# Performance work log

Measured on AMD Instinct MI355X. Metric: run time of the kernel, lower is better.

Reference implementation:

```python
import jax, jax.numpy as jnp
import numpy as np

B = 65536        # batch of class observations
NUM_CLASSES = 100
D = 128          # embedding_latent_dim / MLP width
H = 64           # rnn_hidden_dim == vq_embedding_dim (must match when use_vq)
K = 512          # vq_num_embeddings
S = 16           # num_splines
A = 6            # spline_action_dim
SQUISH = 0.2
BETA = 0.25      # vq commitment cost


def setup_inputs() -> dict:
    key = jax.random.key(0)
    ks = jax.random.split(key, 32)
    g = lambda i, shape, s=0.05: jax.random.normal(ks[i], shape, jnp.float32) * s
    return dict(
        obs=jax.random.randint(ks[0], (B,), 0, NUM_CLASSES, dtype=jnp.int32),
        embed=g(1, (NUM_CLASSES, D)),
        W1=g(2, (D, D)), b1=jnp.zeros((D,), jnp.float32),
        W2=g(3, (D, D)), b2=jnp.zeros((D,), jnp.float32),
        W3=g(4, (D, D)), b3=jnp.zeros((D,), jnp.float32),
        Wc=g(5, (D, H)), bc=jnp.zeros((H,), jnp.float32),      # carry_init
        Wi=g(6, (D, H)), bi=jnp.zeros((H,), jnp.float32),      # SimpleCell input dense
        Wh=g(7, (H, H)),                                       # SimpleCell recurrent (no bias)
        vq_emb=g(8, (K, H)),                                   # VQ codebook
        Wm=g(9, (H, A)), bm=jnp.zeros((A,), jnp.float32),      # actor mean head
        Ws=g(10, (H, A)), bs=jnp.zeros((A,), jnp.float32),     # actor scale head
        Vw1=g(11, (D, D)), vb1=jnp.zeros((D,), jnp.float32),
        Vw2=g(12, (D, D)), vb2=jnp.zeros((D,), jnp.float32),
        Vw3=g(13, (D, 32)), vb3=jnp.zeros((32,), jnp.float32),
        Vw4=g(14, (32, 1)), vb4=jnp.zeros((1,), jnp.float32),
    )


def reference(obs, embed, W1, b1, W2, b2, W3, b3, Wc, bc, Wi, bi, Wh, vq_emb,
              Wm, bm, Ws, bs, Vw1, vb1, Vw2, vb2, Vw3, vb3, Vw4, vb4):
    # class embedding + ReLU MLP trunk
    z = embed[obs]                                # (B, D)
    z = jax.nn.relu(z @ W1 + b1)
    z = jax.nn.relu(z @ W2 + b2)
    z = jax.nn.relu(z @ W3 + b3)

    carry0 = z @ Wc + bc                          # (B, H) initial RNN carry
    emb_sq = jnp.sum(vq_emb ** 2, axis=1)         # (K,) precomputed codebook norms

    def step(carry, _):
        # SimpleCell: h = tanh(Dense(inputs) + Dense_h(carry)); inputs = z each step
        h = jnp.tanh(z @ Wi + bi + carry @ Wh)    # (B, H)
        # VQ nearest-neighbor lookup
        d = jnp.sum(h ** 2, axis=1, keepdims=True) - 2.0 * (h @ vq_emb.T) + emb_sq  # (B, K)
        idx = jnp.argmin(d, axis=1)               # (B,)
        quant = jnp.take(vq_emb, idx, axis=0)     # (B, H) == one_hot(idx) @ vq_emb
        q = h + jax.lax.stop_gradient(quant - h)  # straight-through estimator
        e_loss = jnp.mean((jax.lax.stop_gradient(q) - h) ** 2)
        q_loss = jnp.mean((q - jax.lax.stop_gradient(h)) ** 2)
        vq_loss_i = q_loss + BETA * e_loss
        # spline heads (use_tanh_last=False -> sigmoid, temp=1)
        am = jax.nn.sigmoid(q @ Wm + bm)                    # (B, A)
        sd = jax.nn.sigmoid(q @ Ws + bs) * SQUISH + 1e-8    # (B, A)
        return q, (am, sd, vq_loss_i, idx)

    _, (ams, sds, losses, idxs) = jax.lax.scan(step, carry0, None, length=S)
    # (S, B, A) -> (B, S*A), matching concatenate along axis 1 in step order
    actor_mean = jnp.transpose(ams, (1, 0, 2)).reshape(B, S * A)
    actor_scale_diag = jnp.transpose(sds, (1, 0, 2)).reshape(B, S * A)

    # critic MLP (tanh activations)
    c = jnp.tanh(z @ Vw1 + vb1)
    c = jnp.tanh(c @ Vw2 + vb2)
    c = jnp.tanh(c @ Vw3 + vb3)
    critic = jnp.squeeze(c @ Vw4 + vb4, axis=-1)  # (B,)

    total_vq_loss = jnp.sum(losses)
    return actor_mean, actor_scale_diag, critic, total_vq_loss, idxs
```

## Files before the change

kernel.cpp:

```cpp
#include <hip/hip_runtime.h>
#include <cmath>


#define D_ 128
#define H_ 64
#define K_ 512
#define S_ 16
#define B_ 65536
#define NTBL_ 64
#define NH_ 16

#define OAM   ((size_t)0)
#define OSD   ((size_t)(B_ * 96))
#define OCRIT ((size_t)(2 * B_ * 96))
#define OLOSS ((size_t)(2 * B_ * 96 + B_))
#define OIDX  ((size_t)(2 * B_ * 96 + B_ + 1))

#define WS_CLIDX  0
#define WS_CLAM   (WS_CLIDX + 128 * 16)
#define WS_CLSD   (WS_CLAM + 128 * 96)
#define WS_CLCR   (WS_CLSD + 128 * 96)
#define WS_CLLOSS (WS_CLCR + 128)

__device__ float g_vqwh[K_ * H_];
__device__ float g_am8[K_ * 8];
__device__ float g_sd8[K_ * 8];
__device__ float g_embsq[K_];
__device__ int   g_cntp[NH_ * 128];
__device__ int   g_tflag = 0;

typedef const __attribute__((address_space(1))) void GASV;
typedef __attribute__((address_space(3))) void LASV;
__device__ __forceinline__ void gll16(const void* g, void* l)
{
    __builtin_amdgcn_global_load_lds((GASV*)g, (LASV*)l, 16, 0, 0);
}

template <int N4>
__device__ __forceinline__ void dma_lin(float4* __restrict__ dst,
                                        const float4* __restrict__ src,
                                        int wid, int lane)
{
    constexpr int PER = N4 / 8;
#pragma unroll
    for (int j = 0; j < PER; j += 64) {
        const int f = wid * PER + j;
        gll16(src + f + lane, dst + f);
    }
}

template <int CTRL>
__device__ __forceinline__ void dpp_min(float& bD, int& bK)
{
    const int od_i = __builtin_amdgcn_update_dpp(
        __float_as_int(bD), __float_as_int(bD), CTRL, 0xF, 0xF, false);
    const int ok = __builtin_amdgcn_update_dpp(bK, bK, CTRL, 0xF, 0xF, false);
    const float od = __int_as_float(od_i);
    if (od < bD || (od == bD && ok < bK)) { bD = od; bK = ok; }
}

__global__ __launch_bounds__(512)
__attribute__((amdgpu_waves_per_eu(2, 2)))
void class_kernel(
    const int* __restrict__ obs, int nclass,
    const float* __restrict__ embed,
    const float* __restrict__ W1, const float* __restrict__ b1,
    const float* __restrict__ W2, const float* __restrict__ b2,
    const float* __restrict__ W3, const float* __restrict__ b3,
    const float* __restrict__ Wc, const float* __restrict__ bc,
    const float* __restrict__ Wi, const float* __restrict__ bi,
    const float* __restrict__ Wh,
    const float* __restrict__ Wm, const float* __restrict__ bm,
    const float* __restrict__ Wsw, const float* __restrict__ bs,
    const float* __restrict__ Vw1, const float* __restrict__ vb1,
    const float* __restrict__ Vw2, const float* __restrict__ vb2,
    const float* __restrict__ Vw3, const float* __restrict__ vb3,
    const float* __restrict__ Vw4, const float* __restrict__ vb4,
    const float* __restrict__ vq_emb,
    float* __restrict__ clam, float* __restrict__ clsd,
    float* __restrict__ clcr, float* __restrict__ clidx,
    float* __restrict__ clloss)
{
    extern __shared__ float4 dyn4[];
    float* __restrict__ Af    = reinterpret_cast<float*>(dyn4);
    float* __restrict__ Bf    = reinterpret_cast<float*>(dyn4 + 4096);
    float* __restrict__ vqwhL = reinterpret_cast<float*>(dyn4);
    __shared__ float zA[128], zB[128];
    __shared__ float psum[512];
    __shared__ float psumC[256];
    __shared__ float t1s[64], c0s[64], c3s[32];
    __shared__ float vw4s[32] __attribute__((aligned(16)));
    __shared__ float Wh_s[64 * 64] __attribute__((aligned(16)));
    __shared__ float hcand[2][4][64] __attribute__((aligned(16)));
    __shared__ float rDp[2][4] __attribute__((aligned(16)));
    __shared__ int   rKp[2][4] __attribute__((aligned(16)));
    __shared__ int   gk_s[16];
    __shared__ float gd_s[16];
    __shared__ float hh_s[16];

    const int bx   = blockIdx.x;
    const int tid  = threadIdx.x;
    const int lane = tid & 63;
    const int wid  = tid >> 6;

    if (bx < NTBL_) {
        float* __restrict__ er = reinterpret_cast<float*>(dyn4) + wid * 64;
        const int k = bx * 8 + wid;
        er[lane] = vq_emb[k * 64 + lane];
        __syncthreads();

        float acc = 0.f;
#pragma unroll 16
        for (int dd = 0; dd < 64; ++dd)
            acc = fmaf(er[dd], Wh[dd * 64 + lane], acc);
        g_vqwh[k * 64 + lane] = acc;

        float sq = er[lane] * er[lane];
#pragma unroll
        for (int m = 1; m < 64; m <<= 1) sq += __shfl_xor(sq, m);
        if (lane == 0) g_embsq[k] = sq;

        if (lane < 8) {
            float vm = 0.f, vs = 0.f;
            if (lane < 6) {
                vm = bm[lane];
                vs = bs[lane];
#pragma unroll 16
                for (int dd = 0; dd < 64; ++dd) {
                    vm = fmaf(er[dd], Wm[dd * 6 + lane], vm);
                    vs = fmaf(er[dd], Wsw[dd * 6 + lane], vs);
                }
                vm = 1.f / (1.f + expf(-vm));
                vs = 1.f / (1.f + expf(-vs)) * 0.2f + 1e-8f;
            }
            g_am8[k * 8 + lane] = vm;
            g_sd8[k * 8 + lane] = vs;
        }
        __syncthreads();
        if (tid == 0) {
            __threadfence();
            __hip_atomic_fetch_add(&g_tflag, 1, __ATOMIC_RELEASE,
                                   __HIP_MEMORY_SCOPE_AGENT);
        }
        return;
    }

    if (bx < NTBL_ + NH_) {
        int* __restrict__ hsh = reinterpret_cast<int*>(psum);
        if (tid < 128) hsh[tid] = 0;
        __syncthreads();
        const int hb = bx - NTBL_;
        for (int i = hb * 512 + tid; i < B_; i += NH_ * 512)
            atomicAdd(&hsh[obs[i]], 1);
        __syncthreads();
        if (tid < 128) g_cntp[hb * 128 + tid] = hsh[tid];
        return;
    }

    const int c = bx - NTBL_ - NH_;
    const float4* __restrict__ vq4   = reinterpret_cast<const float4*>(vq_emb);
    const float4* __restrict__ vqwh4 =
        reinterpret_cast<const float4*>(&g_vqwh[0]);

    const int j128 = tid & 127;
    const int q4   = tid >> 7;

    dma_lin<4096>(dyn4, reinterpret_cast<const float4*>(W1), wid, lane);
    if (tid < 128) zA[tid] = embed[c * 128 + tid];
    __syncthreads();

#define DENSE128(SRCW, ZSRC, ZDST, BIAS, ACT)                                  \
    {                                                                          \
        float a0 = 0.f, a1 = 0.f, a2 = 0.f, a3 = 0.f;                          \
        const int i0 = q4 * 32;                                                \
        _Pragma("unroll 8")                                                    \
        for (int ii = 0; ii < 32; ii += 4) {                                   \
            a0 = fmaf(ZSRC[i0 + ii + 0], SRCW[(i0 + ii + 0) * 128 + j128], a0);\
            a1 = fmaf(ZSRC[i0 + ii + 1], SRCW[(i0 + ii + 1) * 128 + j128], a1);\
            a2 = fmaf(ZSRC[i0 + ii + 2], SRCW[(i0 + ii + 2) * 128 + j128], a2);\
            a3 = fmaf(ZSRC[i0 + ii + 3], SRCW[(i0 + ii + 3) * 128 + j128], a3);\
        }                                                                      \
        psum[q4 * 128 + j128] = (a0 + a1) + (a2 + a3);                         \
    }                                                                          \
    __syncthreads();                                                           \
    if (tid < 128) {                                                           \
        float v = BIAS[tid] + ((psum[tid] + psum[128 + tid]) +                 \
                               (psum[256 + tid] + psum[384 + tid]));           \
        ZDST[tid] = ACT;                                                       \
    }                                                                          \
    __syncthreads();

    dma_lin<4096>(dyn4 + 4096, reinterpret_cast<const float4*>(W2), wid, lane);
    DENSE128(Af, zA, zB, b1, fmaxf(v, 0.f))

    dma_lin<4096>(dyn4, reinterpret_cast<const float4*>(W3), wid, lane);
    DENSE128(Bf, zB, zA, b2, fmaxf(v, 0.f))

    dma_lin<2048>(dyn4 + 4096, reinterpret_cast<const float4*>(Wi), wid, lane);
    dma_lin<2048>(dyn4 + 6144, reinterpret_cast<const float4*>(Wc), wid, lane);
    DENSE128(Af, zA, zB, b3, fmaxf(v, 0.f))

    if (tid == 0) {
        while (__hip_atomic_load(&g_tflag, __ATOMIC_RELAXED,
                                 __HIP_MEMORY_SCOPE_AGENT) < NTBL_)
            __builtin_amdgcn_s_sleep(2);
    }
    __syncthreads();

    dma_lin<4096>(dyn4, vqwh4, wid, lane);
    dma_lin<1024>(reinterpret_cast<float4*>(Wh_s),
                  reinterpret_cast<const float4*>(Wh), wid, lane);
    if (wid < 4) {
        const int jj = lane;
        const int qq = wid;
        const int i0 = qq * 32;
        {
            float a0 = 0.f, a1 = 0.f, a2 = 0.f, a3 = 0.f;
#pragma unroll 8
            for (int ii = 0; ii < 32; ii += 4) {
                a0 = fmaf(zB[i0 + ii + 0], Bf[(i0 + ii + 0) * 64 + jj], a0);
                a1 = fmaf(zB[i0 + ii + 1], Bf[(i0 + ii + 1) * 64 + jj], a1);
                a2 = fmaf(zB[i0 + ii + 2], Bf[(i0 + ii + 2) * 64 + jj], a2);
                a3 = fmaf(zB[i0 + ii + 3], Bf[(i0 + ii + 3) * 64 + jj], a3);
            }
            psum[qq * 64 + jj] = (a0 + a1) + (a2 + a3);
        }
        {
            const float* __restrict__ Wsrc = Bf + 8192;
            float a0 = 0.f, a1 = 0.f, a2 = 0.f, a3 = 0.f;
#pragma unroll 8
            for (int ii = 0; ii < 32; ii += 4) {
                a0 = fmaf(zB[i0 + ii + 0], Wsrc[(i0 + ii + 0) * 64 + jj], a0);
                a1 = fmaf(zB[i0 + ii + 1], Wsrc[(i0 + ii + 1) * 64 + jj], a1);
                a2 = fmaf(zB[i0 + ii + 2], Wsrc[(i0 + ii + 2) * 64 + jj], a2);
                a3 = fmaf(zB[i0 + ii + 3], Wsrc[(i0 + ii + 3) * 64 + jj], a3);
            }
            psum[256 + qq * 64 + jj] = (a0 + a1) + (a2 + a3);
        }
    } else {
        const int u = tid - 256;
        const int j = u & 127;
        const int hf = u >> 7;
        const int i0 = 64 * hf;
        float ca0 = 0.f, ca1 = 0.f, ca2 = 0.f, ca3 = 0.f;
#pragma unroll 8
        for (int ii = 0; ii < 64; ii += 4) {
            ca0 = fmaf(zB[i0 + ii + 0], Vw1[(i0 + ii + 0) * 128 + j], ca0);
            ca1 = fmaf(zB[i0 + ii + 1], Vw1[(i0 + ii + 1) * 128 + j], ca1);
            ca2 = fmaf(zB[i0 + ii + 2], Vw1[(i0 + ii + 2) * 128 + j], ca2);
            ca3 = fmaf(zB[i0 + ii + 3], Vw1[(i0 + ii + 3) * 128 + j], ca3);
        }
        psumC[u] = (ca0 + ca1) + (ca2 + ca3);
    }
    __syncthreads();

    dma_lin<4096>(dyn4 + 4096, vqwh4 + 4096, wid, lane);
    if (tid < 64) {
        t1s[tid] = bi[tid] + ((psum[tid] + psum[64 + tid]) +
                              (psum[128 + tid] + psum[192 + tid]));
    } else if (tid < 128) {
        const int j = tid - 64;
        c0s[j] = bc[j] + ((psum[256 + j] + psum[320 + j]) +
                          (psum[384 + j] + psum[448 + j]));
    } else if (tid < 160) {
        vw4s[tid - 128] = Vw4[tid - 128];
    } else if (tid >= 256 && tid < 384) {
        const int u = tid - 256;
        zA[u] = tanhf(vb1[u] + psumC[u] + psumC[128 + u]);
    }
    __syncthreads();

    float4 cb[16], cb2[16];
    float esq = 0.f, esq2 = 0.f;
    if (wid < 4) {
        const int j = lane;
#pragma unroll
        for (int qq2 = 0; qq2 < 2; ++qq2) {
            const int q = wid + 4 * qq2;
            float a0 = 0.f, a1 = 0.f;
            const int i0 = q * 8;
#pragma unroll
            for (int ii = 0; ii < 8; ii += 2) {
                a0 = fmaf(c0s[i0 + ii + 0], Wh_s[(i0 + ii + 0) * 64 + j], a0);
                a1 = fmaf(c0s[i0 + ii + 1], Wh_s[(i0 + ii + 1) * 64 + j], a1);
            }
            psum[q * 64 + j] = a0 + a1;
        }
        const float4* __restrict__ r1 = vq4 + (size_t)tid * 16;
        const float4* __restrict__ r2 = vq4 + (size_t)(tid + 256) * 16;
#pragma unroll
        for (int d4 = 0; d4 < 16; ++d4) { cb[d4] = r1[d4]; cb2[d4] = r2[d4]; }
#pragma unroll
        for (int d4 = 0; d4 < 16; ++d4) {
            asm volatile("" : "+v"(cb[d4].x), "+v"(cb[d4].y),
                              "+v"(cb[d4].z), "+v"(cb[d4].w));
            asm volatile("" : "+v"(cb2[d4].x), "+v"(cb2[d4].y),
                              "+v"(cb2[d4].z), "+v"(cb2[d4].w));
        }
        esq  = g_embsq[tid];
        esq2 = g_embsq[tid + 256];
    } else {
        const int u = tid - 256;
        const int j = u & 127;
        const int hf = u >> 7;
        const int i0 = 64 * hf;
        float ca0 = 0.f, ca1 = 0.f, ca2 = 0.f, ca3 = 0.f;
#pragma unroll 8
        for (int ii = 0; ii < 64; ii += 4) {
            ca0 = fmaf(zA[i0 + ii + 0], Vw2[(i0 + ii + 0) * 128 + j], ca0);
            ca1 = fmaf(zA[i0 + ii + 1], Vw2[(i0 + ii + 1) * 128 + j], ca1);
            ca2 = fmaf(zA[i0 + ii + 2], Vw2[(i0 + ii + 2) * 128 + j], ca2);
            ca3 = fmaf(zA[i0 + ii + 3], Vw2[(i0 + ii + 3) * 128 + j], ca3);
        }
        psumC[u] = (ca0 + ca1) + (ca2 + ca3);
    }
    __syncthreads();

    if (tid < 64) {
        float a = 0.f;
#pragma unroll
        for (int q = 0; q < 8; ++q) a += psum[q * 64 + tid];
        hcand[0][0][tid] = tanhf(a + t1s[tid]);
    } else if (tid >= 256 && tid < 384) {
        const int u = tid - 256;
        zA[u] = tanhf(vb2[u] + psumC[u] + psumC[128 + u]);
    }
    const float t1r = t1s[lane];
    __syncthreads();

    if (wid == 0) {
        const float h0v = hcand[0][0][lane];
        float hh = h0v * h0v;
#pragma unroll
        for (int m = 1; m < 64; m <<= 1) hh += __shfl_xor(hh, m);
        if (lane == 0) hh_s[0] = hh;
    }

    int prevw = 0;
#pragma unroll 1
    for (int t = 0; t < S_; ++t) {
        const int buf = t & 1;
        if (wid < 4) {
            const float* __restrict__ cur = hcand[buf][prevw];
            float a0 = 0.f, a1 = 0.f, a2 = 0.f, a3 = 0.f;
            float b0 = 0.f, b1_ = 0.f, b2_ = 0.f, b3_ = 0.f;
#pragma unroll
            for (int d4 = 0; d4 < 16; d4 += 4) {
                const float4 h0v = *reinterpret_cast<const float4*>(cur + 4 * d4);
                a0 = fmaf(h0v.x, cb[d4].x, a0); a0 = fmaf(h0v.y, cb[d4].y, a0);
                a0 = fmaf(h0v.z, cb[d4].z, a0); a0 = fmaf(h0v.w, cb[d4].w, a0);
                b0 = fmaf(h0v.x, cb2[d4].x, b0); b0 = fmaf(h0v.y, cb2[d4].y, b0);
                b0 = fmaf(h0v.z, cb2[d4].z, b0); b0 = fmaf(h0v.w, cb2[d4].w, b0);
                const float4 h1v = *reinterpret_cast<const float4*>(cur + 4 * d4 + 4);
                a1 = fmaf(h1v.x, cb[d4 + 1].x, a1); a1 = fmaf(h1v.y, cb[d4 + 1].y, a1);
                a1 = fmaf(h1v.z, cb[d4 + 1].z, a1); a1 = fmaf(h1v.w, cb[d4 + 1].w, a1);
                b1_ = fmaf(h1v.x, cb2[d4 + 1].x, b1_); b1_ = fmaf(h1v.y, cb2[d4 + 1].y, b1_);
                b1_ = fmaf(h1v.z, cb2[d4 + 1].z, b1_); b1_ = fmaf(h1v.w, cb2[d4 + 1].w, b1_);
                const float4 h2v = *reinterpret_cast<const float4*>(cur + 4 * d4 + 8);
                a2 = fmaf(h2v.x, cb[d4 + 2].x, a2); a2 = fmaf(h2v.y, cb[d4 + 2].y, a2);
                a2 = fmaf(h2v.z, cb[d4 + 2].z, a2); a2 = fmaf(h2v.w, cb[d4 + 2].w, a2);
                b2_ = fmaf(h2v.x, cb2[d4 + 2].x, b2_); b2_ = fmaf(h2v.y, cb2[d4 + 2].y, b2_);
                b2_ = fmaf(h2v.z, cb2[d4 + 2].z, b2_); b2_ = fmaf(h2v.w, cb2[d4 + 2].w, b2_);
                const float4 h3v = *reinterpret_cast<const float4*>(cur + 4 * d4 + 12);
                a3 = fmaf(h3v.x, cb[d4 + 3].x, a3); a3 = fmaf(h3v.y, cb[d4 + 3].y, a3);
                a3 = fmaf(h3v.z, cb[d4 + 3].z, a3); a3 = fmaf(h3v.w, cb[d4 + 3].w, a3);
                b3_ = fmaf(h3v.x, cb2[d4 + 3].x, b3_); b3_ = fmaf(h3v.y, cb2[d4 + 3].y, b3_);
                b3_ = fmaf(h3v.z, cb2[d4 + 3].z, b3_); b3_ = fmaf(h3v.w, cb2[d4 + 3].w, b3_);
            }
            const float d1 = fmaf(-2.f, (a0 + a1) + (a2 + a3), esq);
            const float d2 = fmaf(-2.f, (b0 + b1_) + (b2_ + b3_), esq2);
            float bD = d1;
            int   bK = tid;
            if (d2 < bD) { bD = d2; bK = tid + 256; }
            dpp_min<0x121>(bD, bK);
            dpp_min<0x122>(bD, bK);
            dpp_min<0x124>(bD, bK);
            dpp_min<0x128>(bD, bK);
            dpp_min<0x142>(bD, bK);
            dpp_min<0x143>(bD, bK);
            const float gDw = __int_as_float(
                __builtin_amdgcn_readlane(__float_as_int(bD), 63));
            const int gKw = __builtin_amdgcn_readlane(bK, 63);
            const float vw = vqwhL[(gKw << 6) + lane];
            hcand[buf ^ 1][wid][lane] = tanhf(t1r + vw);
            if (lane == 0) { rDp[buf][wid] = gDw; rKp[buf][wid] = gKw; }
        } else {
            const int u = tid - 256;
            if (t == 0) {
                const int j2 = u & 31;
                const int o  = u >> 5;
                float x0 = 0.f, x1 = 0.f;
                const int i0 = 16 * o;
#pragma unroll
                for (int ii = 0; ii < 16; ii += 2) {
                    x0 = fmaf(zA[i0 + ii + 0], Vw3[(i0 + ii + 0) * 32 + j2], x0);
                    x1 = fmaf(zA[i0 + ii + 1], Vw3[(i0 + ii + 1) * 32 + j2], x1);
                }
                psumC[u] = x0 + x1;
            } else if (t == 1) {
                if (u < 32) {
                    float v = vb3[u];
#pragma unroll
                    for (int o = 0; o < 8; ++o) v += psumC[o * 32 + u];
                    c3s[u] = tanhf(v);
                }
            } else if (t == 2) {
                if (u == 0) {
                    float sm = vb4[0];
#pragma unroll
                    for (int i = 0; i < 32; ++i) sm = fmaf(c3s[i], vw4s[i], sm);
                    clcr[c] = sm;
                }
            }
        }
        __syncthreads();

        const float4 rd = *reinterpret_cast<const float4*>(&rDp[buf][0]);
        const int4   rk = *reinterpret_cast<const int4*>(&rKp[buf][0]);
        float gD = rd.x;
        int   gK = rk.x, winw = 0;
        if (rd.y < gD || (rd.y == gD && rk.y < gK)) { gD = rd.y; gK = rk.y; winw = 1; }
        if (rd.z < gD || (rd.z == gD && rk.z < gK)) { gD = rd.z; gK = rk.z; winw = 2; }
        if (rd.w < gD || (rd.w == gD && rk.w < gK)) { gD = rd.w; gK = rk.w; winw = 3; }
        if (tid == 0) { gk_s[t] = gK; gd_s[t] = gD; }
        prevw = winw;
    }
    __syncthreads();

    for (int tt = wid + 1; tt < S_; tt += 8) {
        const int g = gk_s[tt - 1];
        const float hv = tanhf(t1r + vqwhL[(g << 6) + lane]);
        float hh = hv * hv;
#pragma unroll
        for (int m = 1; m < 64; m <<= 1) hh += __shfl_xor(hh, m);
        if (lane == 0) hh_s[tt] = hh;
    }
    __syncthreads();
    if (tid == 0) {
        float s = 0.f;
#pragma unroll
        for (int t = 0; t < S_; ++t) s += gd_s[t] + hh_s[t];
        clloss[c] = s;
    }

    if (tid < 96) {
        const int t = tid / 6;
        const int j = tid - t * 6;
        const int gk = gk_s[t];
        clam[c * 96 + tid] = g_am8[gk * 8 + j];
        clsd[c * 96 + tid] = g_sd8[gk * 8 + j];
    } else if (tid >= 96 && tid < 112) {
        const int t = tid - 96;
        clidx[c * 16 + t] = (float)gk_s[t];
    }
}

__global__ __launch_bounds__(256) void scatter_kernel(
    const int* __restrict__ obs, const float* __restrict__ clam,
    const float* __restrict__ clsd, const float* __restrict__ clcr,
    const float* __restrict__ clidx,
    const float* __restrict__ clloss, int nclass, float* __restrict__ out)
{
    __shared__ int icc_s[128];
    if (blockIdx.x == 0) {
        if (threadIdx.x == 0)
            __hip_atomic_store(&g_tflag, 0, __ATOMIC_RELAXED,
                               __HIP_MEMORY_SCOPE_AGENT);
        if (threadIdx.x < 128) {
            int cc = 0;
#pragma unroll
            for (int p = 0; p < NH_; ++p)
                cc += g_cntp[p * 128 + threadIdx.x];
            icc_s[threadIdx.x] = cc;
        }
        __syncthreads();
        if (threadIdx.x == 0) {
            float s = 0.f;
            for (int c = 0; c < nclass; ++c)
                s += (float)icc_s[c] * clloss[c];
            out[OLOSS] = s * 1.25f / (65536.f * 64.f);
        }
    }

    const int n_am4 = B_ * 24;
    const int n_cr4 = B_ / 4;
    const int n_idx = B_ * 16;
    const int tot   = 2 * n_am4 + n_cr4 + n_idx;
    float4* __restrict__ out4 = reinterpret_cast<float4*>(out);

    for (int i = blockIdx.x * 256 + threadIdx.x; i < tot; i += gridDim.x * 256) {
        if (i < 2 * n_am4) {
            const bool in_am = (i < n_am4);
            const int  i4    = in_am ? i : i - n_am4;
            const uint32_t row =
                (uint32_t)(((uint64_t)(i4 >> 3) * 0xAAAAAAABull) >> 33);
            const int col4 = i4 - (int)row * 24;
            const int cc   = obs[row];
            const float* __restrict__ tab = in_am ? clam : clsd;
            out4[i] = *reinterpret_cast<const float4*>(tab + cc * 96 + col4 * 4);
        } else if (i < 2 * n_am4 + n_cr4) {
            const int j = i - 2 * n_am4;
            const int r = 4 * j;
            float4 v;
            v.x = clcr[obs[r + 0]];
            v.y = clcr[obs[r + 1]];
            v.z = clcr[obs[r + 2]];
            v.w = clcr[obs[r + 3]];
            out4[i] = v;
        } else {
            const int j = i - (2 * n_am4 + n_cr4);
            const int t = j >> 16;
            const int r = j & (B_ - 1);
            out[OIDX + (size_t)j] = clidx[obs[r] * 16 + t];
        }
    }
}

extern "C" void kernel_launch(void* const* d_in, const int* in_sizes, int n_in,
                              void* d_out, int out_size, void* d_ws, size_t ws_size,
                              hipStream_t stream)
{
    const int*   obs   = (const int*)  d_in[0];
    const float* embed = (const float*)d_in[1];
    const float* W1    = (const float*)d_in[2];
    const float* b1    = (const float*)d_in[3];
    const float* W2    = (const float*)d_in[4];
    const float* b2    = (const float*)d_in[5];
    const float* W3    = (const float*)d_in[6];
    const float* b3    = (const float*)d_in[7];
    const float* Wc    = (const float*)d_in[8];
    const float* bc    = (const float*)d_in[9];
    const float* Wi    = (const float*)d_in[10];
    const float* bi    = (const float*)d_in[11];
    const float* Wh    = (const float*)d_in[12];
    const float* vq    = (const float*)d_in[13];
    const float* Wm    = (const float*)d_in[14];
    const float* bm    = (const float*)d_in[15];
    const float* Ws    = (const float*)d_in[16];
    const float* bs    = (const float*)d_in[17];
    const float* Vw1   = (const float*)d_in[18];
    const float* vb1   = (const float*)d_in[19];
    const float* Vw2   = (const float*)d_in[20];
    const float* vb2   = (const float*)d_in[21];
    const float* Vw3   = (const float*)d_in[22];
    const float* vb3   = (const float*)d_in[23];
    const float* Vw4   = (const float*)d_in[24];
    const float* vb4   = (const float*)d_in[25];

    const int nclass = in_sizes[1] / D_;

    float* ws_f   = (float*)d_ws;
    float* clidx  = ws_f + WS_CLIDX;
    float* clam   = ws_f + WS_CLAM;
    float* clsd   = ws_f + WS_CLSD;
    float* clcr   = ws_f + WS_CLCR;
    float* clloss = ws_f + WS_CLLOSS;

    float* out = (float*)d_out;

    class_kernel<<<NTBL_ + NH_ + nclass, 512, 131072, stream>>>(
        obs, nclass,
        embed, W1, b1, W2, b2, W3, b3, Wc, bc, Wi, bi, Wh,
        Wm, bm, Ws, bs,
        Vw1, vb1, Vw2, vb2, Vw3, vb3, Vw4, vb4,
        vq,
        clam, clsd, clcr, clidx, clloss);
    scatter_kernel<<<2048, 256, 0, stream>>>(obs, clam, clsd, clcr, clidx,
                                             clloss, nclass, out);
}
```

Measured before the change: 54.68 us.

## Split VQ codebook search across all eight waves and prefetch weights into L2

The per-step nearest-codebook search now uses all 8 waves, one codebook row per thread, instead of 4 waves each handling two rows. The cross-wave reduction grows from 4 to 8 candidates and the hcand/rDp/rKp buffers double. The critic waves still do their small side work inside the loop after the search. A burst of global-to-LDS loads into a scratch region is also added to warm the cache with the weights needed later. This aims to halve the per-thread FMA chain and register pressure in the serial 16-step loop, at the cost of a wider reduction and extra prefetch traffic.

Result: slower. 59.18 us (+8.2%).

```diff
diff --git a/kernel.cpp b/kernel.cpp
--- a/kernel.cpp
+++ b/kernel.cpp
@@ -91,9 +91,9 @@
     __shared__ float t1s[64], c0s[64], c3s[32];
     __shared__ float vw4s[32] __attribute__((aligned(16)));
     __shared__ float Wh_s[64 * 64] __attribute__((aligned(16)));
-    __shared__ float hcand[2][4][64] __attribute__((aligned(16)));
-    __shared__ float rDp[2][4] __attribute__((aligned(16)));
-    __shared__ int   rKp[2][4] __attribute__((aligned(16)));
+    __shared__ float hcand[2][8][64] __attribute__((aligned(16)));
+    __shared__ float rDp[2][8] __attribute__((aligned(16)));
+    __shared__ int   rKp[2][8] __attribute__((aligned(16)));
     __shared__ int   gk_s[16];
     __shared__ float gd_s[16];
     __shared__ float hh_s[16];
@@ -167,6 +167,20 @@
 
     dma_lin<4096>(dyn4, reinterpret_cast<const float4*>(W1), wid, lane);
     if (tid < 128) zA[tid] = embed[c * 128 + tid];
+    {
+        float4* __restrict__ dummy = dyn4 + 4096 + wid * 64;
+        const int gl = tid;
+        gll16(Vw1 + gl * 32, dummy);
+        gll16(Vw2 + gl * 32, dummy);
+        gll16(vq_emb + gl * 32, dummy);
+        gll16(vq_emb + (512 + gl) * 32, dummy);
+        gll16(W2 + gl * 32, dummy);
+        gll16(W3 + gl * 32, dummy);
+        if (wid < 4) gll16(Wi + gl * 32, dummy);
+        else         gll16(Wc + (gl - 256) * 32, dummy);
+        if (wid < 2)      gll16(Wh + gl * 32, dummy);
+        else if (wid < 4) gll16(Vw3 + (gl - 128) * 32, dummy);
+    }
     __syncthreads();
 
 #define DENSE128(SRCW, ZSRC, ZDST, BIAS, ACT)                                  \
@@ -270,8 +284,19 @@
     }
     __syncthreads();
 
-    float4 cb[16], cb2[16];
-    float esq = 0.f, esq2 = 0.f;
+    float4 cb[16];
+    float esq;
+    {
+        const float4* __restrict__ r1 = vq4 + (size_t)tid * 16;
+#pragma unroll
+        for (int d4 = 0; d4 < 16; ++d4) cb[d4] = r1[d4];
+#pragma unroll
+        for (int d4 = 0; d4 < 16; ++d4) {
+            asm volatile("" : "+v"(cb[d4].x), "+v"(cb[d4].y),
+                              "+v"(cb[d4].z), "+v"(cb[d4].w));
+        }
+        esq = g_embsq[tid];
+    }
     if (wid < 4) {
         const int j = lane;
 #pragma unroll
@@ -286,19 +311,6 @@
             }
             psum[q * 64 + j] = a0 + a1;
         }
-        const float4* __restrict__ r1 = vq4 + (size_t)tid * 16;
-        const float4* __restrict__ r2 = vq4 + (size_t)(tid + 256) * 16;
-#pragma unroll
-        for (int d4 = 0; d4 < 16; ++d4) { cb[d4] = r1[d4]; cb2[d4] = r2[d4]; }
-#pragma unroll
-        for (int d4 = 0; d4 < 16; ++d4) {
-            asm volatile("" : "+v"(cb[d4].x), "+v"(cb[d4].y),
-                              "+v"(cb[d4].z), "+v"(cb[d4].w));
-            asm volatile("" : "+v"(cb2[d4].x), "+v"(cb2[d4].y),
-                              "+v"(cb2[d4].z), "+v"(cb2[d4].w));
-        }
-        esq  = g_embsq[tid];
-        esq2 = g_embsq[tid + 256];
     } else {
         const int u = tid - 256;
         const int j = u & 127;
@@ -340,51 +352,39 @@
 #pragma unroll 1
     for (int t = 0; t < S_; ++t) {
         const int buf = t & 1;
-        if (wid < 4) {
-            const float* __restrict__ cur = hcand[buf][prevw];
-            float a0 = 0.f, a1 = 0.f, a2 = 0.f, a3 = 0.f;
-            float b0 = 0.f, b1_ = 0.f, b2_ = 0.f, b3_ = 0.f;
-#pragma unroll
-            for (int d4 = 0; d4 < 16; d4 += 4) {
-                const float4 h0v = *reinterpret_cast<const float4*>(cur + 4 * d4);
-                a0 = fmaf(h0v.x, cb[d4].x, a0); a0 = fmaf(h0v.y, cb[d4].y, a0);
-                a0 = fmaf(h0v.z, cb[d4].z, a0); a0 = fmaf(h0v.w, cb[d4].w, a0);
-                b0 = fmaf(h0v.x, cb2[d4].x, b0); b0 = fmaf(h0v.y, cb2[d4].y, b0);
-                b0 = fmaf(h0v.z, cb2[d4].z, b0); b0 = fmaf(h0v.w, cb2[d4].w, b0);
-                const float4 h1v = *reinterpret_cast<const float4*>(cur + 4 * d4 + 4);
-                a1 = fmaf(h1v.x, cb[d4 + 1].x, a1); a1 = fmaf(h1v.y, cb[d4 + 1].y, a1);
-                a1 = fmaf(h1v.z, cb[d4 + 1].z, a1); a1 = fmaf(h1v.w, cb[d4 + 1].w, a1);
-                b1_ = fmaf(h1v.x, cb2[d4 + 1].x, b1_); b1_ = fmaf(h1v.y, cb2[d4 + 1].y, b1_);
-                b1_ = fmaf(h1v.z, cb2[d4 + 1].z, b1_); b1_ = fmaf(h1v.w, cb2[d4 + 1].w, b1_);
-                const float4 h2v = *reinterpret_cast<const float4*>(cur + 4 * d4 + 8);
-                a2 = fmaf(h2v.x, cb[d4 + 2].x, a2); a2 = fmaf(h2v.y, cb[d4 + 2].y, a2);
-                a2 = fmaf(h2v.z, cb[d4 + 2].z, a2); a2 = fmaf(h2v.w, cb[d4 + 2].w, a2);
-                b2_ = fmaf(h2v.x, cb2[d4 + 2].x, b2_); b2_ = fmaf(h2v.y, cb2[d4 + 2].y, b2_);
-                b2_ = fmaf(h2v.z, cb2[d4 + 2].z, b2_); b2_ = fmaf(h2v.w, cb2[d4 + 2].w, b2_);
-                const float4 h3v = *reinterpret_cast<const float4*>(cur + 4 * d4 + 12);
-                a3 = fmaf(h3v.x, cb[d4 + 3].x, a3); a3 = fmaf(h3v.y, cb[d4 + 3].y, a3);
-                a3 = fmaf(h3v.z, cb[d4 + 3].z, a3); a3 = fmaf(h3v.w, cb[d4 + 3].w, a3);
-                b3_ = fmaf(h3v.x, cb2[d4 + 3].x, b3_); b3_ = fmaf(h3v.y, cb2[d4 + 3].y, b3_);
-                b3_ = fmaf(h3v.z, cb2[d4 + 3].z, b3_); b3_ = fmaf(h3v.w, cb2[d4 + 3].w, b3_);
-            }
-            const float d1 = fmaf(-2.f, (a0 + a1) + (a2 + a3), esq);
-            const float d2 = fmaf(-2.f, (b0 + b1_) + (b2_ + b3_), esq2);
-            float bD = d1;
-            int   bK = tid;
-            if (d2 < bD) { bD = d2; bK = tid + 256; }
-            dpp_min<0x121>(bD, bK);
-            dpp_min<0x122>(bD, bK);
-            dpp_min<0x124>(bD, bK);
-            dpp_min<0x128>(bD, bK);
-            dpp_min<0x142>(bD, bK);
-            dpp_min<0x143>(bD, bK);
-            const float gDw = __int_as_float(
-                __builtin_amdgcn_readlane(__float_as_int(bD), 63));
-            const int gKw = __builtin_amdgcn_readlane(bK, 63);
-            const float vw = vqwhL[(gKw << 6) + lane];
-            hcand[buf ^ 1][wid][lane] = tanhf(t1r + vw);
-            if (lane == 0) { rDp[buf][wid] = gDw; rKp[buf][wid] = gKw; }
-        } else {
+        const float* __restrict__ cur = hcand[buf][prevw];
+        float a0 = 0.f, a1 = 0.f, a2 = 0.f, a3 = 0.f;
+#pragma unroll
+        for (int d4 = 0; d4 < 16; d4 += 4) {
+            const float4 h0v = *reinterpret_cast<const float4*>(cur + 4 * d4);
+            a0 = fmaf(h0v.x, cb[d4].x, a0); a0 = fmaf(h0v.y, cb[d4].y, a0);
+            a0 = fmaf(h0v.z, cb[d4].z, a0); a0 = fmaf(h0v.w, cb[d4].w, a0);
+            const float4 h1v = *reinterpret_cast<const float4*>(cur + 4 * d4 + 4);
+            a1 = fmaf(h1v.x, cb[d4 + 1].x, a1); a1 = fmaf(h1v.y, cb[d4 + 1].y, a1);
+            a1 = fmaf(h1v.z, cb[d4 + 1].z, a1); a1 = fmaf(h1v.w, cb[d4 + 1].w, a1);
+            const float4 h2v = *reinterpret_cast<const float4*>(cur + 4 * d4 + 8);
+            a2 = fmaf(h2v.x, cb[d4 + 2].x, a2); a2 = fmaf(h2v.y, cb[d4 + 2].y, a2);
+            a2 = fmaf(h2v.z, cb[d4 + 2].z, a2); a2 = fmaf(h2v.w, cb[d4 + 2].w, a2);
+            const float4 h3v = *reinterpret_cast<const float4*>(cur + 4 * d4 + 12);
+            a3 = fmaf(h3v.x, cb[d4 + 3].x, a3); a3 = fmaf(h3v.y, cb[d4 + 3].y, a3);
+            a3 = fmaf(h3v.z, cb[d4 + 3].z, a3); a3 = fmaf(h3v.w, cb[d4 + 3].w, a3);
+        }
+        float bD = fmaf(-2.f, (a0 + a1) + (a2 + a3), esq);
+        int   bK = tid;
+        dpp_min<0x121>(bD, bK);
+        dpp_min<0x122>(bD, bK);
+        dpp_min<0x124>(bD, bK);
+        dpp_min<0x128>(bD, bK);
+        dpp_min<0x142>(bD, bK);
+        dpp_min<0x143>(bD, bK);
+        const float gDw = __int_as_float(
+            __builtin_amdgcn_readlane(__float_as_int(bD), 63));
+        const int gKw = __builtin_amdgcn_readlane(bK, 63);
+        const float vw = vqwhL[(gKw << 6) + lane];
+        hcand[buf ^ 1][wid][lane] = tanhf(t1r + vw);
+        if (lane == 0) { rDp[buf][wid] = gDw; rKp[buf][wid] = gKw; }
+
+        if (wid >= 4) {
             const int u = tid - 256;
             if (t == 0) {
                 const int j2 = u & 31;
@@ -415,13 +415,22 @@
         }
         __syncthreads();
 
-        const float4 rd = *reinterpret_cast<const float4*>(&rDp[buf][0]);
-        const int4   rk = *reinterpret_cast<const int4*>(&rKp[buf][0]);
-        float gD = rd.x;
-        int   gK = rk.x, winw = 0;
-        if (rd.y < gD || (rd.y == gD && rk.y < gK)) { gD = rd.y; gK = rk.y; winw = 1; }
-        if (rd.z < gD || (rd.z == gD && rk.z < gK)) { gD = rd.z; gK = rk.z; winw = 2; }
-        if (rd.w < gD || (rd.w == gD && rk.w < gK)) { gD = rd.w; gK = rk.w; winw = 3; }
+        const float4 rd0 = *reinterpret_cast<const float4*>(&rDp[buf][0]);
+        const float4 rd1 = *reinterpret_cast<const float4*>(&rDp[buf][4]);
+        const int4   rk0 = *reinterpret_cast<const int4*>(&rKp[buf][0]);
+        const int4   rk1 = *reinterpret_cast<const int4*>(&rKp[buf][4]);
+        float gD = rd0.x;
+        int   gK = rk0.x, winw = 0;
+#define CMB8(DD, KK, WW) \
+        if (DD < gD || (DD == gD && KK < gK)) { gD = DD; gK = KK; winw = WW; }
+        CMB8(rd0.y, rk0.y, 1)
+        CMB8(rd0.z, rk0.z, 2)
+        CMB8(rd0.w, rk0.w, 3)
+        CMB8(rd1.x, rk1.x, 4)
+        CMB8(rd1.y, rk1.y, 5)
+        CMB8(rd1.z, rk1.z, 6)
+        CMB8(rd1.w, rk1.w, 7)
+#undef CMB8
         if (tid == 0) { gk_s[t] = gK; gd_s[t] = gD; }
         prevw = winw;
     }
```
